# Performance work log

Hardware: AMD Instinct MI355X
Metric: run time of the kernel (lower is better)

The kernel has to match this reference:

```python
import jax, jax.numpy as jnp
import numpy as np
from math import sqrt

D_MODEL = 768
D_T = 256
N_HEADS = 12
HEAD_DIM = D_MODEL // N_HEADS
SCALE = sqrt(HEAD_DIM)


def setup_inputs() -> dict:
    key = jax.random.key(0)
    ks = jax.random.split(key, 11)
    b, l = 8, 1024
    inv = 1.0 / sqrt(D_MODEL)
    inv_t = 1.0 / sqrt(D_T)
    return {
        "x": jax.random.normal(ks[0], (b, l, D_MODEL), dtype=jnp.float32),
        "t": jax.random.normal(ks[1], (b, D_T), dtype=jnp.float32),
        "rel_pos_bias": jax.random.normal(ks[2], (N_HEADS, l, l), dtype=jnp.float32),
        # torch Linear weights: [out_features, in_features]
        "Wx_q": jax.random.normal(ks[3], (D_MODEL, D_MODEL), dtype=jnp.float32) * inv,
        "Wx_k": jax.random.normal(ks[4], (D_MODEL, D_MODEL), dtype=jnp.float32) * inv,
        "Wx_v": jax.random.normal(ks[5], (D_MODEL, D_MODEL), dtype=jnp.float32) * inv,
        "Wt_q": jax.random.normal(ks[6], (D_MODEL, D_T), dtype=jnp.float32) * inv_t,
        "Wt_k": jax.random.normal(ks[7], (D_MODEL, D_T), dtype=jnp.float32) * inv_t,
        "Wt_v": jax.random.normal(ks[8], (D_MODEL, D_T), dtype=jnp.float32) * inv_t,
        "W_o": jax.random.normal(ks[9], (D_MODEL, D_MODEL), dtype=jnp.float32) * inv,
        "b_o": jax.random.normal(ks[10], (D_MODEL,), dtype=jnp.float32) * 0.01,
    }


def _split_heads(y):
    # [b, l, n*d] -> [b, n, l, d]
    b, l, _ = y.shape
    return y.reshape(b, l, N_HEADS, HEAD_DIM).transpose(0, 2, 1, 3)


def reference(x, t, rel_pos_bias, Wx_q, Wx_k, Wx_v, Wt_q, Wt_k, Wt_v, W_o, b_o):
    # time-conditioned QKV: per-batch additive shift broadcast over seq
    q = _split_heads(x @ Wx_q.T + (t @ Wt_q.T)[:, None, :])
    k = _split_heads(x @ Wx_k.T + (t @ Wt_k.T)[:, None, :])
    v = _split_heads(x @ Wx_v.T + (t @ Wt_v.T)[:, None, :])
    attn = jnp.einsum("bnld,bnmd->bnlm", q, k) / SCALE
    attn = attn + rel_pos_bias  # [n,l,l] broadcasts over batch
    probs = jax.nn.softmax(attn, axis=-1)
    o = jnp.einsum("bnlm,bnmd->bnld", probs, v)
    b, _, l, _ = o.shape
    o = o.transpose(0, 2, 1, 3).reshape(b, l, D_MODEL)
    return o @ W_o.T + b_o
```

## Files before the change

kernel.cpp:

```cpp
#include <hip/hip_runtime.h>
#include <hip/hip_bf16.h>
#include <stdint.h>

typedef __bf16 bf16_t;
typedef __attribute__((ext_vector_type(8))) __bf16 bf16x8;
typedef __attribute__((ext_vector_type(4))) __bf16 bf16x4;
typedef __attribute__((ext_vector_type(4))) float f32x4;

#define DEVI __device__ __forceinline__

DEVI void gll16(const void* g, void* lds_base_wave_uniform) {
  __builtin_amdgcn_global_load_lds(
      (const __attribute__((address_space(1))) uint32_t*)(uintptr_t)g,
      (__attribute__((address_space(3))) uint32_t*)(uintptr_t)lds_base_wave_uniform,
      16, 0, 0);
}

__global__ void cvt_f32_to_bf16(const float* __restrict__ src, bf16_t* __restrict__ dst, int n) {
  int i = (blockIdx.x * blockDim.x + threadIdx.x) * 4;
  if (i >= n) return;
  float4 v = *(const float4*)(src + i);
  bf16x4 o = {(bf16_t)v.x, (bf16_t)v.y, (bf16_t)v.z, (bf16_t)v.w};
  *(bf16x4*)(dst + i) = o;
}

__global__ void shift_kernel(const float* __restrict__ t,
                             const float* __restrict__ wtq,
                             const float* __restrict__ wtk,
                             const float* __restrict__ wtv,
                             float* __restrict__ shift) {
  int idx = blockIdx.x * blockDim.x + threadIdx.x;
  if (idx >= 8 * 2304) return;
  int b = idx / 2304, n = idx % 2304;
  const float* w = (n < 768) ? (wtq + (size_t)n * 256)
                 : (n < 1536) ? (wtk + (size_t)(n - 768) * 256)
                              : (wtv + (size_t)(n - 1536) * 256);
  const float4* tv = (const float4*)(t + (size_t)b * 256);
  const float4* wv = (const float4*)w;
  float acc = 0.f;
#pragma unroll 8
  for (int i = 0; i < 64; i++) {
    float4 a = tv[i], c = wv[i];
    acc += a.x * c.x + a.y * c.y + a.z * c.z + a.w * c.w;
  }
  shift[idx] = acc;
}

template <int MODE>
__global__ __launch_bounds__(256, 2) void gemm_bt(
    const bf16_t* __restrict__ A, const bf16_t* __restrict__ B,
    const float* __restrict__ add, void* __restrict__ Cout,
    int M, int N, int K) {
  __shared__ alignas(16) bf16_t As[128 * 32];
  __shared__ alignas(16) bf16_t Bs[128 * 32];
  const int t = threadIdx.x, l = t & 63, w = t >> 6;
  const int wr = w >> 1, wc = w & 1;
  const int bm = blockIdx.x, bn = blockIdx.y;

  f32x4 acc[4][4] = {};

  const int srow = t >> 2;
  const int scol = (t & 3) * 8;
  const bf16_t* Ab = A + ((size_t)bm * 128 + srow) * K + scol;
  const bf16_t* Bb = B + ((size_t)bn * 128 + srow) * K + scol;
  char* AsB = (char*)As + w * 1024;
  char* BsB = (char*)Bs + w * 1024;
  const size_t K64 = (size_t)64 * K;

  const int ro = (l & 15) * 32 + (l >> 4) * 8;
  const bf16_t* ApA = As + (wr * 64) * 32 + ro;
  const bf16_t* BpB = Bs + (wc * 64) * 32 + ro;

  for (int k0 = 0; k0 < K; k0 += 32) {
    __syncthreads();
    gll16(Ab + k0, AsB);
    gll16(Ab + K64 + k0, AsB + 4096);
    gll16(Bb + k0, BsB);
    gll16(Bb + K64 + k0, BsB + 4096);
    __syncthreads();
    bf16x8 af[4], bfr[4];
#pragma unroll
    for (int i = 0; i < 4; i++) {
      af[i]  = *(const bf16x8*)(ApA + i * 16 * 32);
      bfr[i] = *(const bf16x8*)(BpB + i * 16 * 32);
    }
#pragma unroll
    for (int mi = 0; mi < 4; mi++)
#pragma unroll
      for (int ni = 0; ni < 4; ni++)
        acc[mi][ni] = __builtin_amdgcn_mfma_f32_16x16x32_bf16(af[mi], bfr[ni], acc[mi][ni], 0, 0, 0);
  }

  const int row0 = bm * 128 + wr * 64 + (l >> 4) * 4;
  const int col0 = bn * 128 + wc * 64 + (l & 15);
  if (MODE == 0) {
    bf16_t* C = (bf16_t*)Cout;
    const float* sh = add + (size_t)((bm * 128) >> 10) * N;
#pragma unroll
    for (int ni = 0; ni < 4; ni++) {
      const int col = col0 + ni * 16;
      const float s0 = sh[col];
#pragma unroll
      for (int mi = 0; mi < 4; mi++)
#pragma unroll
        for (int i = 0; i < 4; i++)
          C[(size_t)(row0 + mi * 16 + i) * N + col] = (bf16_t)(acc[mi][ni][i] + s0);
    }
  } else {
    float* C = (float*)Cout;
#pragma unroll
    for (int ni = 0; ni < 4; ni++) {
      const int col = col0 + ni * 16;
      const float s0 = add[col];
#pragma unroll
      for (int mi = 0; mi < 4; mi++)
#pragma unroll
        for (int i = 0; i < 4; i++)
          C[(size_t)(row0 + mi * 16 + i) * N + col] = acc[mi][ni][i] + s0;
    }
  }
}

__global__ __launch_bounds__(256, 2) void attn_fused(
    const bf16_t* __restrict__ qkv,
    const bf16_t* __restrict__ bias,
    bf16_t* __restrict__ o) {
  const int qt = blockIdx.x, h = blockIdx.y, b = blockIdx.z;
  const int t = threadIdx.x, l = t & 63, w = t >> 6;

  __shared__ alignas(16) bf16_t Ks[64 * 64];
  __shared__ alignas(16) bf16_t Vt[64 * 64];
  __shared__ alignas(16) bf16_t Bi[64 * 64];
  __shared__ alignas(16) bf16_t Ps[4][16 * 64];

  const size_t rowb = (size_t)b * 1024;

  bf16x8 qf[2];
  {
    const bf16_t* qp = qkv + (rowb + qt * 64 + w * 16 + (l & 15)) * 2304 + h * 64 + (l >> 4) * 8;
    qf[0] = *(const bf16x8*)qp;
    qf[1] = *(const bf16x8*)(qp + 32);
  }

  float m_run[4] = {-INFINITY, -INFINITY, -INFINITY, -INFINITY};
  float l_run[4] = {0.f, 0.f, 0.f, 0.f};
  f32x4 oacc[4] = {};

  const int sr = t >> 3;
  const int sc = t & 7;
  char* KsB = (char*)Ks + w * 1024;
  char* BiB = (char*)Bi + w * 1024;
  const float LOG2E = 1.44269504088896f;

  for (int kt = 0; kt < 16; kt++) {
    __syncthreads();
#pragma unroll
    for (int s = 0; s < 2; s++) {
      const int r = s * 32 + sr;
      const int gc = (sc ^ (r & 7)) * 8;
      gll16(qkv + (rowb + kt * 64 + r) * 2304 + 768 + h * 64 + gc, KsB + s * 4096);
      gll16(bias + ((size_t)h * 1024 + qt * 64 + r) * 1024 + kt * 64 + gc, BiB + s * 4096);
    }
    {
      const bf16_t* vp = qkv + (rowb + kt * 64 + l) * 2304 + 1536 + h * 64 + w * 16;
      bf16x8 v0 = *(const bf16x8*)vp;
      bf16x8 v1 = *(const bf16x8*)(vp + 8);
#pragma unroll
      for (int j = 0; j < 16; j++) {
        const int d = w * 16 + j;
        const int addr = d * 64 + (((l >> 3) ^ (d & 7)) * 8) + (l & 7);
        Vt[addr] = (j < 8) ? v0[j] : v1[j - 8];
      }
    }
    __syncthreads();

    f32x4 sv[4];
#pragma unroll
    for (int nf = 0; nf < 4; nf++) {
      const int kp = nf * 16 + (l & 15);
      const bf16_t* kb = Ks + kp * 64;
      bf16x8 kf0 = *(const bf16x8*)(kb + (((l >> 4) ^ (kp & 7)) * 8));
      bf16x8 kf1 = *(const bf16x8*)(kb + ((((l >> 4) + 4) ^ (kp & 7)) * 8));
      f32x4 z = {0.f, 0.f, 0.f, 0.f};
      z = __builtin_amdgcn_mfma_f32_16x16x32_bf16(qf[0], kf0, z, 0, 0, 0);
      z = __builtin_amdgcn_mfma_f32_16x16x32_bf16(qf[1], kf1, z, 0, 0, 0);
      sv[nf] = z;
    }

    float p[4][4];
    float alpha[4];
#pragma unroll
    for (int i = 0; i < 4; i++) {
      const int r = w * 16 + (l >> 4) * 4 + i;
      float lg[4];
#pragma unroll
      for (int nf = 0; nf < 4; nf++) {
        const int kp = nf * 16 + (l & 15);
        const int ba = r * 64 + (((kp >> 3) ^ (r & 7)) * 8) + (kp & 7);
        lg[nf] = sv[nf][i] * 0.125f + (float)Bi[ba];
      }
      float mx = fmaxf(fmaxf(lg[0], lg[1]), fmaxf(lg[2], lg[3]));
      mx = fmaxf(mx, __shfl_xor(mx, 1));
      mx = fmaxf(mx, __shfl_xor(mx, 2));
      mx = fmaxf(mx, __shfl_xor(mx, 4));
      mx = fmaxf(mx, __shfl_xor(mx, 8));
      const float mnew = fmaxf(m_run[i], mx);
      alpha[i] = exp2f((m_run[i] - mnew) * LOG2E);
      m_run[i] = mnew;
      float rs = 0.f;
#pragma unroll
      for (int nf = 0; nf < 4; nf++) {
        p[nf][i] = exp2f((lg[nf] - mnew) * LOG2E);
        rs += p[nf][i];
      }
      rs += __shfl_xor(rs, 1);
      rs += __shfl_xor(rs, 2);
      rs += __shfl_xor(rs, 4);
      rs += __shfl_xor(rs, 8);
      l_run[i] = l_run[i] * alpha[i] + rs;
    }

    bf16_t* Pw = Ps[w];
#pragma unroll
    for (int nf = 0; nf < 4; nf++)
#pragma unroll
      for (int i = 0; i < 4; i++) {
        const int rq = (l >> 4) * 4 + i;
        const int kp = nf * 16 + (l & 15);
        Pw[rq * 64 + (((kp >> 3) ^ (rq & 7)) * 8) + (kp & 7)] = (bf16_t)p[nf][i];
      }
#pragma unroll
    for (int nf2 = 0; nf2 < 4; nf2++)
#pragma unroll
      for (int i = 0; i < 4; i++)
        oacc[nf2][i] *= alpha[i];

    bf16x8 pf[2];
#pragma unroll
    for (int kc = 0; kc < 2; kc++) {
      const int rq = l & 15;
      const int chunk = kc * 4 + (l >> 4);
      pf[kc] = *(const bf16x8*)(Pw + rq * 64 + ((chunk ^ (rq & 7)) * 8));
    }
#pragma unroll
    for (int nf2 = 0; nf2 < 4; nf2++) {
      const int d = nf2 * 16 + (l & 15);
      const bf16_t* vb = Vt + d * 64;
      bf16x8 vf0 = *(const bf16x8*)(vb + (((l >> 4) ^ (d & 7)) * 8));
      bf16x8 vf1 = *(const bf16x8*)(vb + ((((l >> 4) + 4) ^ (d & 7)) * 8));
      oacc[nf2] = __builtin_amdgcn_mfma_f32_16x16x32_bf16(pf[0], vf0, oacc[nf2], 0, 0, 0);
      oacc[nf2] = __builtin_amdgcn_mfma_f32_16x16x32_bf16(pf[1], vf1, oacc[nf2], 0, 0, 0);
    }
  }

#pragma unroll
  for (int i = 0; i < 4; i++) {
    const float inv = 1.0f / l_run[i];
    const size_t row = rowb + qt * 64 + w * 16 + (l >> 4) * 4 + i;
#pragma unroll
    for (int nf2 = 0; nf2 < 4; nf2++)
      o[row * 768 + h * 64 + nf2 * 16 + (l & 15)] = (bf16_t)(oacc[nf2][i] * inv);
  }
}

extern "C" void kernel_launch(void* const* d_in, const int* in_sizes, int n_in,
                              void* d_out, int out_size, void* d_ws, size_t ws_size,
                              hipStream_t stream) {
  const float* x    = (const float*)d_in[0];
  const float* tin  = (const float*)d_in[1];
  const float* bias = (const float*)d_in[2];
  const float* Wxq  = (const float*)d_in[3];
  const float* Wxk  = (const float*)d_in[4];
  const float* Wxv  = (const float*)d_in[5];
  const float* Wtq  = (const float*)d_in[6];
  const float* Wtk  = (const float*)d_in[7];
  const float* Wtv  = (const float*)d_in[8];
  const float* Wo   = (const float*)d_in[9];
  const float* bo   = (const float*)d_in[10];
  float* out = (float*)d_out;

  char* ws = (char*)d_ws;
  bf16_t* x_bf    = (bf16_t*)(ws);
  bf16_t* wcat    = (bf16_t*)(ws + 12582912);
  bf16_t* wo_bf   = (bf16_t*)(ws + 16121856);
  bf16_t* bias_bf = (bf16_t*)(ws + 17301504);
  float*  shift   = (float*) (ws + 42467328);
  bf16_t* qkvb    = (bf16_t*)(ws + 42541056);
  bf16_t* obuf    = (bf16_t*)(ws + 80289792);

  const int W = 768 * 768;
  cvt_f32_to_bf16<<<6144, 256, 0, stream>>>(x, x_bf, 8192 * 768);
  cvt_f32_to_bf16<<<576, 256, 0, stream>>>(Wxq, wcat, W);
  cvt_f32_to_bf16<<<576, 256, 0, stream>>>(Wxk, wcat + W, W);
  cvt_f32_to_bf16<<<576, 256, 0, stream>>>(Wxv, wcat + 2 * W, W);
  cvt_f32_to_bf16<<<576, 256, 0, stream>>>(Wo, wo_bf, W);
  cvt_f32_to_bf16<<<12288, 256, 0, stream>>>(bias, bias_bf, 12 * 1024 * 1024);
  shift_kernel<<<72, 256, 0, stream>>>(tin, Wtq, Wtk, Wtv, shift);
  gemm_bt<0><<<dim3(64, 18), 256, 0, stream>>>(x_bf, wcat, shift, qkvb, 8192, 2304, 768);
  attn_fused<<<dim3(16, 12, 8), 256, 0, stream>>>(qkvb, bias_bf, obuf);
  gemm_bt<1><<<dim3(64, 6), 256, 0, stream>>>(obuf, wo_bf, bo, out, 8192, 768, 768);
}
```

Measured before the change: 343.5 us.

## Read fp32 bias and K fragments directly from global in attention, drop bias conversion

Removes the separate fp32-to-bf16 conversion pass over the 48MB relative position bias. The attention kernel now reads fp32 bias values and K MFMA fragments straight from global memory into registers instead of staging them through LDS. It also remaps the block index so that consecutive blocks share a query tile across head and batch groups, which should improve L2 reuse of the bias. The softmax scaling is folded into one fma in the log2 domain, and one barrier is moved later in the loop. The cost is uncoalesced, strided scalar bias loads, twice the bias bytes per attention block, and more register pressure from holding the K fragments.

```diff
diff --git a/kernel.cpp b/kernel.cpp
--- a/kernel.cpp
+++ b/kernel.cpp
@@ -123,14 +123,16 @@
 
 __global__ __launch_bounds__(256, 2) void attn_fused(
     const bf16_t* __restrict__ qkv,
-    const bf16_t* __restrict__ bias,
+    const float* __restrict__ bias,
     bf16_t* __restrict__ o) {
-  const int qt = blockIdx.x, h = blockIdx.y, b = blockIdx.z;
+  const int id = blockIdx.x;
+  const int slot = id >> 3;
+  const int qt = slot & 15;
+  const int grp = (id & 7) + 8 * (slot >> 4);
+  const int h = grp % 12, b = grp / 12;
   const int t = threadIdx.x, l = t & 63, w = t >> 6;
 
-  __shared__ alignas(16) bf16_t Ks[64 * 64];
   __shared__ alignas(16) bf16_t Vt[64 * 64];
-  __shared__ alignas(16) bf16_t Bi[64 * 64];
   __shared__ alignas(16) bf16_t Ps[4][16 * 64];
 
   const size_t rowb = (size_t)b * 1024;
@@ -142,25 +144,39 @@
     qf[1] = *(const bf16x8*)(qp + 32);
   }
 
+  const float* bbase = bias + ((size_t)h << 20)
+                     + (size_t)(qt * 64 + w * 16 + (l >> 4) * 4) * 1024 + (l & 15);
+  const bf16_t* kbase = qkv + rowb * 2304 + 768 + h * 64 + (l >> 4) * 8;
+
   float m_run[4] = {-INFINITY, -INFINITY, -INFINITY, -INFINITY};
   float l_run[4] = {0.f, 0.f, 0.f, 0.f};
   f32x4 oacc[4] = {};
 
-  const int sr = t >> 3;
-  const int sc = t & 7;
-  char* KsB = (char*)Ks + w * 1024;
-  char* BiB = (char*)Bi + w * 1024;
   const float LOG2E = 1.44269504088896f;
+  const float C1 = 0.125f * 1.44269504088896f;
 
   for (int kt = 0; kt < 16; kt++) {
+    bf16x8 kf[4][2];
+    {
+      const bf16_t* kb = kbase + (size_t)(kt * 64) * 2304;
+#pragma unroll
+      for (int nf = 0; nf < 4; nf++) {
+        const bf16_t* kr = kb + (size_t)(nf * 16 + (l & 15)) * 2304;
+        kf[nf][0] = *(const bf16x8*)kr;
+        kf[nf][1] = *(const bf16x8*)(kr + 32);
+      }
+    }
+    float barr[4][4];
+    {
+      const float* bb = bbase + kt * 64;
+#pragma unroll
+      for (int i = 0; i < 4; i++)
+#pragma unroll
+        for (int nf = 0; nf < 4; nf++)
+          barr[i][nf] = bb[(size_t)i * 1024 + nf * 16];
+    }
+
     __syncthreads();
-#pragma unroll
-    for (int s = 0; s < 2; s++) {
-      const int r = s * 32 + sr;
-      const int gc = (sc ^ (r & 7)) * 8;
-      gll16(qkv + (rowb + kt * 64 + r) * 2304 + 768 + h * 64 + gc, KsB + s * 4096);
-      gll16(bias + ((size_t)h * 1024 + qt * 64 + r) * 1024 + kt * 64 + gc, BiB + s * 4096);
-    }
     {
       const bf16_t* vp = qkv + (rowb + kt * 64 + l) * 2304 + 1536 + h * 64 + w * 16;
       bf16x8 v0 = *(const bf16x8*)vp;
@@ -172,18 +188,13 @@
         Vt[addr] = (j < 8) ? v0[j] : v1[j - 8];
       }
     }
-    __syncthreads();
 
     f32x4 sv[4];
 #pragma unroll
     for (int nf = 0; nf < 4; nf++) {
-      const int kp = nf * 16 + (l & 15);
-      const bf16_t* kb = Ks + kp * 64;
-      bf16x8 kf0 = *(const bf16x8*)(kb + (((l >> 4) ^ (kp & 7)) * 8));
-      bf16x8 kf1 = *(const bf16x8*)(kb + ((((l >> 4) + 4) ^ (kp & 7)) * 8));
       f32x4 z = {0.f, 0.f, 0.f, 0.f};
-      z = __builtin_amdgcn_mfma_f32_16x16x32_bf16(qf[0], kf0, z, 0, 0, 0);
-      z = __builtin_amdgcn_mfma_f32_16x16x32_bf16(qf[1], kf1, z, 0, 0, 0);
+      z = __builtin_amdgcn_mfma_f32_16x16x32_bf16(qf[0], kf[nf][0], z, 0, 0, 0);
+      z = __builtin_amdgcn_mfma_f32_16x16x32_bf16(qf[1], kf[nf][1], z, 0, 0, 0);
       sv[nf] = z;
     }
 
@@ -191,26 +202,22 @@
     float alpha[4];
 #pragma unroll
     for (int i = 0; i < 4; i++) {
-      const int r = w * 16 + (l >> 4) * 4 + i;
       float lg[4];
 #pragma unroll
-      for (int nf = 0; nf < 4; nf++) {
-        const int kp = nf * 16 + (l & 15);
-        const int ba = r * 64 + (((kp >> 3) ^ (r & 7)) * 8) + (kp & 7);
-        lg[nf] = sv[nf][i] * 0.125f + (float)Bi[ba];
-      }
+      for (int nf = 0; nf < 4; nf++)
+        lg[nf] = fmaf(sv[nf][i], C1, barr[i][nf] * LOG2E);
       float mx = fmaxf(fmaxf(lg[0], lg[1]), fmaxf(lg[2], lg[3]));
       mx = fmaxf(mx, __shfl_xor(mx, 1));
       mx = fmaxf(mx, __shfl_xor(mx, 2));
       mx = fmaxf(mx, __shfl_xor(mx, 4));
       mx = fmaxf(mx, __shfl_xor(mx, 8));
       const float mnew = fmaxf(m_run[i], mx);
-      alpha[i] = exp2f((m_run[i] - mnew) * LOG2E);
+      alpha[i] = exp2f(m_run[i] - mnew);
       m_run[i] = mnew;
       float rs = 0.f;
 #pragma unroll
       for (int nf = 0; nf < 4; nf++) {
-        p[nf][i] = exp2f((lg[nf] - mnew) * LOG2E);
+        p[nf][i] = exp2f(lg[nf] - mnew);
         rs += p[nf][i];
       }
       rs += __shfl_xor(rs, 1);
@@ -234,6 +241,8 @@
 #pragma unroll
       for (int i = 0; i < 4; i++)
         oacc[nf2][i] *= alpha[i];
+
+    __syncthreads();
 
     bf16x8 pf[2];
 #pragma unroll
@@ -283,10 +292,9 @@
   bf16_t* x_bf    = (bf16_t*)(ws);
   bf16_t* wcat    = (bf16_t*)(ws + 12582912);
   bf16_t* wo_bf   = (bf16_t*)(ws + 16121856);
-  bf16_t* bias_bf = (bf16_t*)(ws + 17301504);
-  float*  shift   = (float*) (ws + 42467328);
-  bf16_t* qkvb    = (bf16_t*)(ws + 42541056);
-  bf16_t* obuf    = (bf16_t*)(ws + 80289792);
+  float*  shift   = (float*) (ws + 17301504);
+  bf16_t* qkvb    = (bf16_t*)(ws + 17375232);
+  bf16_t* obuf    = (bf16_t*)(ws + 55123968);
 
   const int W = 768 * 768;
   cvt_f32_to_bf16<<<6144, 256, 0, stream>>>(x, x_bf, 8192 * 768);
@@ -294,9 +302,8 @@
   cvt_f32_to_bf16<<<576, 256, 0, stream>>>(Wxk, wcat + W, W);
   cvt_f32_to_bf16<<<576, 256, 0, stream>>>(Wxv, wcat + 2 * W, W);
   cvt_f32_to_bf16<<<576, 256, 0, stream>>>(Wo, wo_bf, W);
-  cvt_f32_to_bf16<<<12288, 256, 0, stream>>>(bias, bias_bf, 12 * 1024 * 1024);
   shift_kernel<<<72, 256, 0, stream>>>(tin, Wtq, Wtk, Wtv, shift);
   gemm_bt<0><<<dim3(64, 18), 256, 0, stream>>>(x_bf, wcat, shift, qkvb, 8192, 2304, 768);
-  attn_fused<<<dim3(16, 12, 8), 256, 0, stream>>>(qkvb, bias_bf, obuf);
+  attn_fused<<<1536, 256, 0, stream>>>(qkvb, bias, obuf);
   gemm_bt<1><<<dim3(64, 6), 256, 0, stream>>>(obuf, wo_bf, bo, out, 8192, 768, 768);
 }
```

New measurement: 344.7 us. About the same (+0.3%).
